# Performance work log

Measured on AMD Instinct MI355X. Metric: run time of the kernel, lower is better.

## Reference

```python
import jax, jax.numpy as jnp
import numpy as np

D_MODEL = 128
NUM_HEADS = 4
D_HEAD = 32
ATTN_COEFF = 0.5
BATCH = 2
SEQ = 4096


def setup_inputs() -> dict:
    key = jax.random.key(0)
    k1, k2, k3, k4, k5 = jax.random.split(key, 5)
    std = 1.0 / np.sqrt(D_MODEL)
    x = jax.random.normal(k1, (BATCH, SEQ, D_MODEL), dtype=jnp.float32)
    W_K = jax.random.normal(k2, (NUM_HEADS, D_HEAD, D_MODEL), dtype=jnp.float32) * std
    W_Q = jax.random.normal(k3, (NUM_HEADS, D_HEAD, D_MODEL), dtype=jnp.float32) * std
    W_V = jax.random.normal(k4, (NUM_HEADS, D_HEAD, D_MODEL), dtype=jnp.float32) * std
    W_O = jax.random.normal(k5, (D_MODEL, NUM_HEADS * D_HEAD), dtype=jnp.float32) * std
    return {"x": x, "W_K": W_K, "W_Q": W_Q, "W_V": W_V, "W_O": W_O}


def reference(x, W_K, W_Q, W_V, W_O):
    batch, seq, _ = x.shape
    # projections: [B, H, S, Dh]
    k = jnp.einsum('ihd,bpd->biph', W_K, x)
    q = jnp.einsum('ihd,bpd->biph', W_Q, x)
    v = jnp.einsum('ihd,bpd->biph', W_V, x)
    # scores: [B, H, Sq, Sk]
    scores = jnp.einsum('biph,biqh->biqp', k, q) / np.sqrt(D_HEAD).astype(np.float32)
    # NOTE: original code builds a causal mask but never applies it; faithful omission.
    attn = jax.nn.softmax(scores, axis=-1)
    # post-softmax affine blend with uniform offset
    attn = attn * ATTN_COEFF + (1.0 - ATTN_COEFF)
    z = jnp.einsum('biph,biqp->biqh', v, attn)          # [B, H, S, Dh]
    z_flat = jnp.transpose(z, (0, 2, 1, 3)).reshape(batch, seq, NUM_HEADS * D_HEAD)
    out = jnp.einsum('df,bpf->bpd', W_O, z_flat)        # [B, S, D]
    return out
```

## Files before the change

kernel.cpp:

```cpp
#include <hip/hip_runtime.h>

#define SQ 4096
#define NB 2
#define NH 4
#define DH 32
#define DM 128

typedef float f32x16 __attribute__((ext_vector_type(16)));
typedef float f32x4  __attribute__((ext_vector_type(4)));
typedef __bf16 bf16x8 __attribute__((ext_vector_type(8)));
typedef unsigned int uint4v __attribute__((ext_vector_type(4)));
typedef unsigned short u16;

union B8 { uint4v u; bf16x8 b; };

__device__ inline u16 f2bf(float x) {
  unsigned u = __builtin_bit_cast(unsigned, x);
  unsigned r = (u + 0x7FFF + ((u >> 16) & 1)) >> 16;
  return (u16)r;
}

__device__ inline unsigned cvt_pk_bf16(float a, float b) {
  unsigned r;
  asm("v_cvt_pk_bf16_f32 %0, %1, %2" : "=v"(r) : "v"(a), "v"(b));
  return r;
}

__device__ inline void swap32(unsigned &a, unsigned &b) {
  asm("v_permlane32_swap_b32 %0, %1" : "+v"(a), "+v"(b));
}

#if __has_builtin(__builtin_amdgcn_exp2f)
#define EX2 __builtin_amdgcn_exp2f
#else
#define EX2 exp2f
#endif

__device__ inline float xhalf_add(float x) {
  unsigned ua = __builtin_bit_cast(unsigned, x), ub = ua;
  asm("v_permlane32_swap_b32 %0, %1" : "+v"(ua), "+v"(ub));
  return __builtin_bit_cast(float, ua) + __builtin_bit_cast(float, ub);
}

__device__ inline bf16x8 ld_cvt8(const float* p) {
  f32x4 a = *(const f32x4*)p;
  f32x4 b = *(const f32x4*)(p + 4);
  B8 r;
  r.u[0] = cvt_pk_bf16(a[0], a[1]);
  r.u[1] = cvt_pk_bf16(a[2], a[3]);
  r.u[2] = cvt_pk_bf16(b[0], b[1]);
  r.u[3] = cvt_pk_bf16(b[2], b[3]);
  return r.b;
}

__global__ __launch_bounds__(256) void kprep(const float* __restrict__ x,
                                             const float* __restrict__ Wo,
                                             u16* __restrict__ wob,
                                             float* __restrict__ xsum) {
  const int bid = blockIdx.x, t = threadIdx.x;
  if (bid < 256) {
    const int b = bid >> 7, rblk = bid & 127;
    const int d = t & 127, rh = t >> 7;
    const float* xp = x + ((size_t)b * SQ + rblk * 32) * DM + d;
    float a = 0.f;
    for (int r = rh; r < 32; r += 2) a += xp[(size_t)r * DM];
    __shared__ float red[2][DM];
    red[rh][d] = a;
    __syncthreads();
    if (t < DM) atomicAdd(&xsum[b * DM + t], red[0][t] + red[1][t]);
  } else {
    for (int i = t; i < DM * DM; i += 256) wob[i] = f2bf(Wo[i]);
  }
}

__global__ __launch_bounds__(256) void kprojc(const float* __restrict__ x,
                                              const float* __restrict__ Wk,
                                              const float* __restrict__ Wq,
                                              const float* __restrict__ Wv,
                                              const float* __restrict__ Wo,
                                              const float* __restrict__ xsum,
                                              u16* __restrict__ qb,
                                              u16* __restrict__ kb,
                                              u16* __restrict__ vt,
                                              float* __restrict__ cvec) {
  const int by = blockIdx.y;
  const int t = threadIdx.x;
  if (by == 12) {
    if (blockIdx.x >= NB) return;
    const int b = blockIdx.x;
    __shared__ float xs[DM], vs[DM];
    if (t < DM) xs[t] = xsum[b * DM + t];
    __syncthreads();
    const int c = t >> 1, half = t & 1;
    float a = 0.f;
    const float* wr = Wv + c * DM + half * 64;
    const float* xh = xs + half * 64;
    for (int i = 0; i < 64; ++i) a += wr[i] * xh[i];
    a += __shfl_xor(a, 1, 64);
    if (half == 0) vs[c] = a;
    __syncthreads();
    float a2 = 0.f;
    const float* wr2 = Wo + c * DM + half * 64;
    const float* vh = vs + half * 64;
    for (int i = 0; i < 64; ++i) a2 += wr2[i] * vh[i];
    a2 += __shfl_xor(a2, 1, 64);
    if (half == 0) cvec[b * DM + c] = 0.5f * a2;
    return;
  }
  const int lane = t & 63, wid = t >> 6;
  const int l31 = lane & 31, hi = lane >> 5;
  const int mat = by >> 2, h = by & 3;
  const int p0 = (blockIdx.x * 4 + wid) * 32;
  const float* xrow = x + (size_t)(p0 + l31) * DM + 8 * hi;
  const float* W = (mat == 0) ? Wk : (mat == 1 ? Wq : Wv);
  const float* wrow = W + (h * 32 + l31) * DM + 8 * hi;
  f32x16 acc;
#pragma unroll
  for (int r = 0; r < 16; ++r) acc[r] = 0.f;
#pragma unroll
  for (int ks = 0; ks < 8; ++ks) {
    bf16x8 af = ld_cvt8(xrow + ks * 16);
    bf16x8 wf = ld_cvt8(wrow + ks * 16);
    acc = __builtin_amdgcn_mfma_f32_32x32x16_bf16(af, wf, acc, 0, 0, 0);
  }
  const float QS = 1.4426950408889634f / 5.656854249492380f;
  const int b = p0 >> 12, pl = p0 & (SQ - 1);
  const size_t bh = (size_t)b * NH + h;
  if (mat == 0) {
    u16* dst = kb + (bh * SQ + pl) * DH + l31;
#pragma unroll
    for (int r = 0; r < 16; ++r) {
      int row = (r & 3) + 8 * (r >> 2) + 4 * hi;
      dst[(size_t)row * DH] = f2bf(acc[r]);
    }
  } else if (mat == 1) {
    u16* dst = qb + (bh * SQ + pl) * DH + l31;
#pragma unroll
    for (int r = 0; r < 16; ++r) {
      int row = (r & 3) + 8 * (r >> 2) + 4 * hi;
      dst[(size_t)row * DH] = f2bf(acc[r] * QS);
    }
  } else {
    u16* dst = vt + ((bh * (SQ / 32) + (pl >> 5)) * DH + l31) * 32;
#pragma unroll
    for (int r = 0; r < 16; ++r) {
      int row = (r & 3) + 8 * (r >> 2) + 4 * hi;
      dst[row] = f2bf(acc[r]);
    }
  }
}

#define TILE(K0, K1, V0, V1, NOFF) {                                               \
  __builtin_amdgcn_s_setprio(1);                                                   \
  f32x16 sc = __builtin_amdgcn_mfma_f32_32x32x16_bf16(K0.b, qf0.b, zacc, 0, 0, 0); \
  sc = __builtin_amdgcn_mfma_f32_32x32x16_bf16(K1.b, qf1.b, sc, 0, 0, 0);          \
  __builtin_amdgcn_s_setprio(0);                                                   \
  K0.u = *(const uint4v*)(kT + (NOFF));                                            \
  K1.u = *(const uint4v*)(kT + (NOFF) + 16);                                       \
  float p_[16];                                                                    \
  _Pragma("unroll") for (int r = 0; r < 16; ++r) p_[r] = EX2(sc[r]);               \
  float ls = ((p_[0]+p_[1])+(p_[2]+p_[3]))+((p_[4]+p_[5])+(p_[6]+p_[7]));          \
  ls += ((p_[8]+p_[9])+(p_[10]+p_[11]))+((p_[12]+p_[13])+(p_[14]+p_[15]));         \
  s += ls;                                                                         \
  unsigned w0 = cvt_pk_bf16(p_[0], p_[1]),  w1 = cvt_pk_bf16(p_[2], p_[3]);        \
  unsigned w2 = cvt_pk_bf16(p_[4], p_[5]),  w3 = cvt_pk_bf16(p_[6], p_[7]);        \
  unsigned w4 = cvt_pk_bf16(p_[8], p_[9]),  w5 = cvt_pk_bf16(p_[10], p_[11]);      \
  unsigned w6 = cvt_pk_bf16(p_[12], p_[13]), w7 = cvt_pk_bf16(p_[14], p_[15]);     \
  swap32(w0, w2); swap32(w1, w3); swap32(w4, w6); swap32(w5, w7);                  \
  B8 bp0_, bp1_;                                                                   \
  bp0_.u[0] = w0; bp0_.u[1] = w1; bp0_.u[2] = w2; bp0_.u[3] = w3;                  \
  bp1_.u[0] = w4; bp1_.u[1] = w5; bp1_.u[2] = w6; bp1_.u[3] = w7;                  \
  __builtin_amdgcn_s_setprio(1);                                                   \
  acc = __builtin_amdgcn_mfma_f32_32x32x16_bf16(V0.b, bp0_.b, acc, 0, 0, 0);       \
  acc = __builtin_amdgcn_mfma_f32_32x32x16_bf16(V1.b, bp1_.b, acc, 0, 0, 0);       \
  __builtin_amdgcn_s_setprio(0);                                                   \
  V0.u = *(const uint4v*)(vT + (NOFF));                                            \
  V1.u = *(const uint4v*)(vT + (NOFF) + 16);                                       \
}

__global__ __launch_bounds__(256, 4) void kattn(const u16* __restrict__ qb,
                                                const u16* __restrict__ kb,
                                                const u16* __restrict__ vt,
                                                u16* __restrict__ yb) {
  __shared__ float ss_[3][64], sa_[3][16][64];
  const int t = threadIdx.x, lane = t & 63, wid = t >> 6;
  const int l31 = lane & 31, hi = lane >> 5;
  const int bh = blockIdx.x & 7;
  const int qbase = (blockIdx.x >> 3) * 32;

  const u16* qrow = qb + ((size_t)bh * SQ + qbase + l31) * DH + 8 * hi;
  B8 qf0, qf1;
  qf0.u = *(const uint4v*)(qrow);
  qf1.u = *(const uint4v*)(qrow + 16);

  const int kh = wid;
  const u16* kT = kb + ((size_t)bh * SQ + kh * 1024) * DH + l31 * 32 + 8 * hi;
  const u16* vT = vt + ((size_t)bh * (SQ / 32) + kh * 32) * (DH * 32) + l31 * 32 + 8 * hi;

  f32x16 zacc, acc;
#pragma unroll
  for (int r = 0; r < 16; ++r) { zacc[r] = -16.f; acc[r] = 0.f; }
  float s = 0.f;

  B8 ka0, ka1, va0, va1, kb0, kb1, vb0, vb1;
  ka0.u = *(const uint4v*)(kT);        ka1.u = *(const uint4v*)(kT + 16);
  va0.u = *(const uint4v*)(vT);        va1.u = *(const uint4v*)(vT + 16);
  kb0.u = *(const uint4v*)(kT + 1024); kb1.u = *(const uint4v*)(kT + 1024 + 16);
  vb0.u = *(const uint4v*)(vT + 1024); vb1.u = *(const uint4v*)(vT + 1024 + 16);

  for (int ti = 0; ti < 32; ti += 2) {
    const int off = ti << 10;
    TILE(ka0, ka1, va0, va1, off + 2048)
    TILE(kb0, kb1, vb0, vb1, off + 3072)
  }

  s = xhalf_add(s);

  if (wid) {
    const int w = wid - 1;
    ss_[w][lane] = s;
#pragma unroll
    for (int r = 0; r < 16; ++r) sa_[w][r][lane] = acc[r];
  }
  __syncthreads();
  if (wid == 0) {
    float den = s;
#pragma unroll
    for (int w = 0; w < 3; ++w) den += ss_[w][lane];
    float inv = 0.5f / den;
    const int b = bh >> 2, h = bh & 3;
    u16* yp = yb + ((size_t)(b * SQ) + qbase + l31) * DM + h * 32;
#pragma unroll
    for (int r = 0; r < 16; ++r) {
      float o = acc[r];
#pragma unroll
      for (int w = 0; w < 3; ++w) o += sa_[w][r][lane];
      int row = (r & 3) + 8 * (r >> 2) + 4 * hi;
      yp[row] = f2bf(o * inv);
    }
  }
}

__global__ __launch_bounds__(256) void kout(const u16* __restrict__ yb,
                                            const u16* __restrict__ wob,
                                            const float* __restrict__ cvec,
                                            float* __restrict__ out) {
  const int t = threadIdx.x, lane = t & 63, wid = t >> 6;
  const int l31 = lane & 31, hi = lane >> 5;
  const int blk = blockIdx.x;
  const int b = blk >> 7;
  const int p0 = (blk & 127) * 32;
  const int d0 = wid * 32;
  const u16* yrow = yb + ((size_t)(b * SQ) + p0 + l31) * DM + 8 * hi;
  const u16* wrow = wob + (size_t)(d0 + l31) * DM + 8 * hi;
  f32x16 acc;
#pragma unroll
  for (int r = 0; r < 16; ++r) acc[r] = 0.f;
#pragma unroll
  for (int ks = 0; ks < 8; ++ks) {
    B8 a, w;
    a.u = *(const uint4v*)(yrow + ks * 16);
    w.u = *(const uint4v*)(wrow + ks * 16);
    acc = __builtin_amdgcn_mfma_f32_32x32x16_bf16(a.b, w.b, acc, 0, 0, 0);
  }
  float cv = cvec[b * DM + d0 + l31];
  float* op = out + ((size_t)(b * SQ) + p0) * DM + d0 + l31;
#pragma unroll
  for (int r = 0; r < 16; ++r) {
    int row = (r & 3) + 8 * (r >> 2) + 4 * hi;
    op[(size_t)row * DM] = acc[r] + cv;
  }
}

extern "C" void kernel_launch(void* const* d_in, const int* in_sizes, int n_in,
                              void* d_out, int out_size, void* d_ws, size_t ws_size,
                              hipStream_t stream) {
  const float* x  = (const float*)d_in[0];
  const float* Wk = (const float*)d_in[1];
  const float* Wq = (const float*)d_in[2];
  const float* Wv = (const float*)d_in[3];
  const float* Wo = (const float*)d_in[4];
  float* out = (float*)d_out;
  char* ws = (char*)d_ws;
  float* xsum = (float*)(ws);
  float* cvec = (float*)(ws + (4 << 10));
  u16* wob = (u16*)(ws + (64 << 10));
  u16* qb = (u16*)(ws + (256 << 10));
  u16* kb = (u16*)(ws + (256 << 10) + ((size_t)2 << 20));
  u16* vt = (u16*)(ws + (256 << 10) + ((size_t)4 << 20));
  u16* yb = (u16*)(ws + (256 << 10) + ((size_t)6 << 20));

  hipMemsetAsync(xsum, 0, NB * DM * sizeof(float), stream);
  kprep<<<dim3(257), dim3(256), 0, stream>>>(x, Wo, wob, xsum);
  kprojc<<<dim3(64, 13), dim3(256), 0, stream>>>(x, Wk, Wq, Wv, Wo, xsum, qb, kb, vt, cvec);
  kattn<<<dim3(1024), dim3(256), 0, stream>>>(qb, kb, vt, yb);
  kout<<<dim3(256), dim3(256), 0, stream>>>(yb, wob, cvec, out);
}
```

Measured before the change: 131.7 us.

## Process two 32-row query tiles per attention block to reuse K/V loads

Each attention block now handles 64 query rows as two 32-row groups that share the same K and V fragments. Each loaded K/V register tile feeds twice the MFMA work, which halves global K/V traffic per query and halves the grid to 512 blocks. In exchange, each thread holds more registers (two accumulators, four Q fragments) and the cross-wave reduction needs twice the shared memory. Fewer blocks on a large GPU may also lower occupancy and parallelism.

```diff
diff --git a/kernel.cpp b/kernel.cpp
--- a/kernel.cpp
+++ b/kernel.cpp
@@ -150,30 +150,37 @@
   }
 }
 
+#define SMPV(SC, S, ACC, V0, V1) {                                              \
+  float p_[16];                                                                 \
+  _Pragma("unroll") for (int r = 0; r < 16; ++r) p_[r] = EX2(SC[r]);            \
+  float ls = ((p_[0]+p_[1])+(p_[2]+p_[3]))+((p_[4]+p_[5])+(p_[6]+p_[7]));       \
+  ls += ((p_[8]+p_[9])+(p_[10]+p_[11]))+((p_[12]+p_[13])+(p_[14]+p_[15]));      \
+  S += ls;                                                                      \
+  unsigned w0 = cvt_pk_bf16(p_[0], p_[1]),  w1 = cvt_pk_bf16(p_[2], p_[3]);     \
+  unsigned w2 = cvt_pk_bf16(p_[4], p_[5]),  w3 = cvt_pk_bf16(p_[6], p_[7]);     \
+  unsigned w4 = cvt_pk_bf16(p_[8], p_[9]),  w5 = cvt_pk_bf16(p_[10], p_[11]);   \
+  unsigned w6 = cvt_pk_bf16(p_[12], p_[13]), w7 = cvt_pk_bf16(p_[14], p_[15]);  \
+  swap32(w0, w2); swap32(w1, w3); swap32(w4, w6); swap32(w5, w7);               \
+  B8 bp0_, bp1_;                                                                \
+  bp0_.u[0] = w0; bp0_.u[1] = w1; bp0_.u[2] = w2; bp0_.u[3] = w3;               \
+  bp1_.u[0] = w4; bp1_.u[1] = w5; bp1_.u[2] = w6; bp1_.u[3] = w7;               \
+  __builtin_amdgcn_s_setprio(1);                                                \
+  ACC = __builtin_amdgcn_mfma_f32_32x32x16_bf16(V0.b, bp0_.b, ACC, 0, 0, 0);    \
+  ACC = __builtin_amdgcn_mfma_f32_32x32x16_bf16(V1.b, bp1_.b, ACC, 0, 0, 0);    \
+  __builtin_amdgcn_s_setprio(0);                                                \
+}
+
 #define TILE(K0, K1, V0, V1, NOFF) {                                               \
   __builtin_amdgcn_s_setprio(1);                                                   \
-  f32x16 sc = __builtin_amdgcn_mfma_f32_32x32x16_bf16(K0.b, qf0.b, zacc, 0, 0, 0); \
-  sc = __builtin_amdgcn_mfma_f32_32x32x16_bf16(K1.b, qf1.b, sc, 0, 0, 0);          \
+  f32x16 sc0 = __builtin_amdgcn_mfma_f32_32x32x16_bf16(K0.b, qf00.b, zacc, 0,0,0); \
+  sc0 = __builtin_amdgcn_mfma_f32_32x32x16_bf16(K1.b, qf01.b, sc0, 0, 0, 0);       \
+  f32x16 sc1 = __builtin_amdgcn_mfma_f32_32x32x16_bf16(K0.b, qf10.b, zacc, 0,0,0); \
+  sc1 = __builtin_amdgcn_mfma_f32_32x32x16_bf16(K1.b, qf11.b, sc1, 0, 0, 0);       \
   __builtin_amdgcn_s_setprio(0);                                                   \
   K0.u = *(const uint4v*)(kT + (NOFF));                                            \
   K1.u = *(const uint4v*)(kT + (NOFF) + 16);                                       \
-  float p_[16];                                                                    \
-  _Pragma("unroll") for (int r = 0; r < 16; ++r) p_[r] = EX2(sc[r]);               \
-  float ls = ((p_[0]+p_[1])+(p_[2]+p_[3]))+((p_[4]+p_[5])+(p_[6]+p_[7]));          \
-  ls += ((p_[8]+p_[9])+(p_[10]+p_[11]))+((p_[12]+p_[13])+(p_[14]+p_[15]));         \
-  s += ls;                                                                         \
-  unsigned w0 = cvt_pk_bf16(p_[0], p_[1]),  w1 = cvt_pk_bf16(p_[2], p_[3]);        \
-  unsigned w2 = cvt_pk_bf16(p_[4], p_[5]),  w3 = cvt_pk_bf16(p_[6], p_[7]);        \
-  unsigned w4 = cvt_pk_bf16(p_[8], p_[9]),  w5 = cvt_pk_bf16(p_[10], p_[11]);      \
-  unsigned w6 = cvt_pk_bf16(p_[12], p_[13]), w7 = cvt_pk_bf16(p_[14], p_[15]);     \
-  swap32(w0, w2); swap32(w1, w3); swap32(w4, w6); swap32(w5, w7);                  \
-  B8 bp0_, bp1_;                                                                   \
-  bp0_.u[0] = w0; bp0_.u[1] = w1; bp0_.u[2] = w2; bp0_.u[3] = w3;                  \
-  bp1_.u[0] = w4; bp1_.u[1] = w5; bp1_.u[2] = w6; bp1_.u[3] = w7;                  \
-  __builtin_amdgcn_s_setprio(1);                                                   \
-  acc = __builtin_amdgcn_mfma_f32_32x32x16_bf16(V0.b, bp0_.b, acc, 0, 0, 0);       \
-  acc = __builtin_amdgcn_mfma_f32_32x32x16_bf16(V1.b, bp1_.b, acc, 0, 0, 0);       \
-  __builtin_amdgcn_s_setprio(0);                                                   \
+  SMPV(sc0, s0, acc0, V0, V1)                                                      \
+  SMPV(sc1, s1, acc1, V0, V1)                                                      \
   V0.u = *(const uint4v*)(vT + (NOFF));                                            \
   V1.u = *(const uint4v*)(vT + (NOFF) + 16);                                       \
 }
@@ -182,25 +189,28 @@
                                                 const u16* __restrict__ kb,
                                                 const u16* __restrict__ vt,
                                                 u16* __restrict__ yb) {
-  __shared__ float ss_[3][64], sa_[3][16][64];
+  __shared__ float ss_[3][2][64], sa_[3][2][16][64];
   const int t = threadIdx.x, lane = t & 63, wid = t >> 6;
   const int l31 = lane & 31, hi = lane >> 5;
   const int bh = blockIdx.x & 7;
-  const int qbase = (blockIdx.x >> 3) * 32;
-
-  const u16* qrow = qb + ((size_t)bh * SQ + qbase + l31) * DH + 8 * hi;
-  B8 qf0, qf1;
-  qf0.u = *(const uint4v*)(qrow);
-  qf1.u = *(const uint4v*)(qrow + 16);
+  const int qbase = (blockIdx.x >> 3) * 64;
+
+  const u16* qrow0 = qb + ((size_t)bh * SQ + qbase + l31) * DH + 8 * hi;
+  const u16* qrow1 = qrow0 + 32 * DH;
+  B8 qf00, qf01, qf10, qf11;
+  qf00.u = *(const uint4v*)(qrow0);
+  qf01.u = *(const uint4v*)(qrow0 + 16);
+  qf10.u = *(const uint4v*)(qrow1);
+  qf11.u = *(const uint4v*)(qrow1 + 16);
 
   const int kh = wid;
   const u16* kT = kb + ((size_t)bh * SQ + kh * 1024) * DH + l31 * 32 + 8 * hi;
   const u16* vT = vt + ((size_t)bh * (SQ / 32) + kh * 32) * (DH * 32) + l31 * 32 + 8 * hi;
 
-  f32x16 zacc, acc;
-#pragma unroll
-  for (int r = 0; r < 16; ++r) { zacc[r] = -16.f; acc[r] = 0.f; }
-  float s = 0.f;
+  f32x16 zacc, acc0, acc1;
+#pragma unroll
+  for (int r = 0; r < 16; ++r) { zacc[r] = -16.f; acc0[r] = 0.f; acc1[r] = 0.f; }
+  float s0 = 0.f, s1 = 0.f;
 
   B8 ka0, ka1, va0, va1, kb0, kb1, vb0, vb1;
   ka0.u = *(const uint4v*)(kT);        ka1.u = *(const uint4v*)(kT + 16);
@@ -214,29 +224,33 @@
     TILE(kb0, kb1, vb0, vb1, off + 3072)
   }
 
-  s = xhalf_add(s);
+  s0 = xhalf_add(s0);
+  s1 = xhalf_add(s1);
 
   if (wid) {
     const int w = wid - 1;
-    ss_[w][lane] = s;
-#pragma unroll
-    for (int r = 0; r < 16; ++r) sa_[w][r][lane] = acc[r];
+    ss_[w][0][lane] = s0; ss_[w][1][lane] = s1;
+#pragma unroll
+    for (int r = 0; r < 16; ++r) { sa_[w][0][r][lane] = acc0[r]; sa_[w][1][r][lane] = acc1[r]; }
   }
   __syncthreads();
   if (wid == 0) {
-    float den = s;
-#pragma unroll
-    for (int w = 0; w < 3; ++w) den += ss_[w][lane];
-    float inv = 0.5f / den;
     const int b = bh >> 2, h = bh & 3;
-    u16* yp = yb + ((size_t)(b * SQ) + qbase + l31) * DM + h * 32;
-#pragma unroll
-    for (int r = 0; r < 16; ++r) {
-      float o = acc[r];
-#pragma unroll
-      for (int w = 0; w < 3; ++w) o += sa_[w][r][lane];
-      int row = (r & 3) + 8 * (r >> 2) + 4 * hi;
-      yp[row] = f2bf(o * inv);
+#pragma unroll
+    for (int g = 0; g < 2; ++g) {
+      float den = g ? s1 : s0;
+#pragma unroll
+      for (int w = 0; w < 3; ++w) den += ss_[w][g][lane];
+      float inv = 0.5f / den;
+      u16* yp = yb + ((size_t)(b * SQ) + qbase + g * 32 + l31) * DM + h * 32;
+#pragma unroll
+      for (int r = 0; r < 16; ++r) {
+        float o = (g ? acc1[r] : acc0[r]);
+#pragma unroll
+        for (int w = 0; w < 3; ++w) o += sa_[w][g][r][lane];
+        int row = (r & 3) + 8 * (r >> 2) + 4 * hi;
+        yp[row] = f2bf(o * inv);
+      }
     }
   }
 }
@@ -293,6 +307,6 @@
   hipMemsetAsync(xsum, 0, NB * DM * sizeof(float), stream);
   kprep<<<dim3(257), dim3(256), 0, stream>>>(x, Wo, wob, xsum);
   kprojc<<<dim3(64, 13), dim3(256), 0, stream>>>(x, Wk, Wq, Wv, Wo, xsum, qb, kb, vt, cvec);
-  kattn<<<dim3(1024), dim3(256), 0, stream>>>(qb, kb, vt, yb);
+  kattn<<<dim3(512), dim3(256), 0, stream>>>(qb, kb, vt, yb);
   kout<<<dim3(256), dim3(256), 0, stream>>>(yb, wob, cvec, out);
 }
```

Result: slower. 346.5 us (+163.2%).

## Share K/V tiles across four query waves via double-buffered LDS async loads

Applied to the files above, without the earlier changes.

Each block now takes 128 queries, one 32-query slice per wave, instead of splitting the key range of 32 queries across waves. K and V tiles are staged into double-buffered LDS with global_load_lds using a swizzled layout, so all four waves reuse each tile. This removes the cross-wave reduction of partial sums through LDS and cuts global K/V traffic by four. The cost is a block-wide barrier every tile, a grid of 256 blocks instead of 1024 (lower occupancy and parallelism), and LDS read latency sitting on the MFMA path.

```diff
diff --git a/kernel.cpp b/kernel.cpp
--- a/kernel.cpp
+++ b/kernel.cpp
@@ -12,6 +12,9 @@
 typedef unsigned int uint4v __attribute__((ext_vector_type(4)));
 typedef unsigned short u16;
 
+#define AS1 __attribute__((address_space(1)))
+#define AS3 __attribute__((address_space(3)))
+
 union B8 { uint4v u; bf16x8 b; };
 
 __device__ inline u16 f2bf(float x) {
@@ -40,6 +43,10 @@
   unsigned ua = __builtin_bit_cast(unsigned, x), ub = ua;
   asm("v_permlane32_swap_b32 %0, %1" : "+v"(ua), "+v"(ub));
   return __builtin_bit_cast(float, ua) + __builtin_bit_cast(float, ub);
+}
+
+__device__ inline void gload16(const void* g, void* l) {
+  __builtin_amdgcn_global_load_lds((const AS1 void*)g, (AS3 void*)l, 16, 0, 0);
 }
 
 __device__ inline bf16x8 ld_cvt8(const float* p) {
@@ -150,13 +157,24 @@
   }
 }
 
-#define TILE(K0, K1, V0, V1, NOFF) {                                               \
+#define STAGE(T, B) {                                              \
+  const char* kg_ = kgbase + (size_t)(T) * 8192;                   \
+  const char* vg_ = vgbase + (size_t)(T) * 8192;                   \
+  gload16(kg_,        &klds[B][woff]);                             \
+  gload16(kg_ + 1024, &klds[B][woff + 1024]);                      \
+  gload16(vg_,        &vlds[B][woff]);                             \
+  gload16(vg_ + 1024, &vlds[B][woff + 1024]);                      \
+}
+
+#define SUB(S) {                                                                   \
+  const int off_ = (S)*2048 + lbase;                                               \
+  B8 k0_, k1_;                                                                     \
+  k0_.u = *(const uint4v*)(kl + off_ + kx0);                                       \
+  k1_.u = *(const uint4v*)(kl + off_ + kx1);                                       \
   __builtin_amdgcn_s_setprio(1);                                                   \
-  f32x16 sc = __builtin_amdgcn_mfma_f32_32x32x16_bf16(K0.b, qf0.b, zacc, 0, 0, 0); \
-  sc = __builtin_amdgcn_mfma_f32_32x32x16_bf16(K1.b, qf1.b, sc, 0, 0, 0);          \
+  f32x16 sc = __builtin_amdgcn_mfma_f32_32x32x16_bf16(k0_.b, qf0.b, zacc, 0,0,0);  \
+  sc = __builtin_amdgcn_mfma_f32_32x32x16_bf16(k1_.b, qf1.b, sc, 0, 0, 0);         \
   __builtin_amdgcn_s_setprio(0);                                                   \
-  K0.u = *(const uint4v*)(kT + (NOFF));                                            \
-  K1.u = *(const uint4v*)(kT + (NOFF) + 16);                                       \
   float p_[16];                                                                    \
   _Pragma("unroll") for (int r = 0; r < 16; ++r) p_[r] = EX2(sc[r]);               \
   float ls = ((p_[0]+p_[1])+(p_[2]+p_[3]))+((p_[4]+p_[5])+(p_[6]+p_[7]));          \
@@ -170,74 +188,66 @@
   B8 bp0_, bp1_;                                                                   \
   bp0_.u[0] = w0; bp0_.u[1] = w1; bp0_.u[2] = w2; bp0_.u[3] = w3;                  \
   bp1_.u[0] = w4; bp1_.u[1] = w5; bp1_.u[2] = w6; bp1_.u[3] = w7;                  \
+  B8 v0_, v1_;                                                                     \
+  v0_.u = *(const uint4v*)(vl + off_ + kx0);                                       \
+  v1_.u = *(const uint4v*)(vl + off_ + kx1);                                       \
   __builtin_amdgcn_s_setprio(1);                                                   \
-  acc = __builtin_amdgcn_mfma_f32_32x32x16_bf16(V0.b, bp0_.b, acc, 0, 0, 0);       \
-  acc = __builtin_amdgcn_mfma_f32_32x32x16_bf16(V1.b, bp1_.b, acc, 0, 0, 0);       \
+  acc = __builtin_amdgcn_mfma_f32_32x32x16_bf16(v0_.b, bp0_.b, acc, 0, 0, 0);      \
+  acc = __builtin_amdgcn_mfma_f32_32x32x16_bf16(v1_.b, bp1_.b, acc, 0, 0, 0);      \
   __builtin_amdgcn_s_setprio(0);                                                   \
-  V0.u = *(const uint4v*)(vT + (NOFF));                                            \
-  V1.u = *(const uint4v*)(vT + (NOFF) + 16);                                       \
-}
-
-__global__ __launch_bounds__(256, 4) void kattn(const u16* __restrict__ qb,
-                                                const u16* __restrict__ kb,
-                                                const u16* __restrict__ vt,
-                                                u16* __restrict__ yb) {
-  __shared__ float ss_[3][64], sa_[3][16][64];
+}
+
+__global__ __launch_bounds__(256) void kattn(const u16* __restrict__ qb,
+                                             const u16* __restrict__ kb,
+                                             const u16* __restrict__ vt,
+                                             u16* __restrict__ yb) {
+  __shared__ char klds[2][8192];
+  __shared__ char vlds[2][8192];
   const int t = threadIdx.x, lane = t & 63, wid = t >> 6;
   const int l31 = lane & 31, hi = lane >> 5;
   const int bh = blockIdx.x & 7;
-  const int qbase = (blockIdx.x >> 3) * 32;
+  const int qbase = (blockIdx.x >> 3) * 128 + wid * 32;
 
   const u16* qrow = qb + ((size_t)bh * SQ + qbase + l31) * DH + 8 * hi;
   B8 qf0, qf1;
   qf0.u = *(const uint4v*)(qrow);
   qf1.u = *(const uint4v*)(qrow + 16);
 
-  const int kh = wid;
-  const u16* kT = kb + ((size_t)bh * SQ + kh * 1024) * DH + l31 * 32 + 8 * hi;
-  const u16* vT = vt + ((size_t)bh * (SQ / 32) + kh * 32) * (DH * 32) + l31 * 32 + 8 * hi;
+  const int srcswz = ((lane >> 2) * 64) + ((((lane & 3) ^ ((lane >> 3) & 3))) << 4);
+  const int woff = wid * 2048;
+  const char* kgbase = (const char*)(kb + (size_t)bh * SQ * DH) + woff + srcswz;
+  const char* vgbase = (const char*)(vt + (size_t)bh * (SQ / 32) * DH * 32) + woff + srcswz;
+
+  const int x_ = (l31 >> 1) & 3;
+  const int kx0 = (hi ^ x_) << 4;
+  const int kx1 = ((2 + hi) ^ x_) << 4;
+  const int lbase = l31 * 64;
 
   f32x16 zacc, acc;
 #pragma unroll
   for (int r = 0; r < 16; ++r) { zacc[r] = -16.f; acc[r] = 0.f; }
   float s = 0.f;
 
-  B8 ka0, ka1, va0, va1, kb0, kb1, vb0, vb1;
-  ka0.u = *(const uint4v*)(kT);        ka1.u = *(const uint4v*)(kT + 16);
-  va0.u = *(const uint4v*)(vT);        va1.u = *(const uint4v*)(vT + 16);
-  kb0.u = *(const uint4v*)(kT + 1024); kb1.u = *(const uint4v*)(kT + 1024 + 16);
-  vb0.u = *(const uint4v*)(vT + 1024); vb1.u = *(const uint4v*)(vT + 1024 + 16);
-
-  for (int ti = 0; ti < 32; ti += 2) {
-    const int off = ti << 10;
-    TILE(ka0, ka1, va0, va1, off + 2048)
-    TILE(kb0, kb1, vb0, vb1, off + 3072)
+  STAGE(0, 0)
+  __syncthreads();
+
+  for (int ti = 0; ti < 32; ++ti) {
+    const int cur = ti & 1;
+    if (ti + 1 < 32) STAGE(ti + 1, cur ^ 1)
+    const char* kl = klds[cur];
+    const char* vl = vlds[cur];
+    SUB(0) SUB(1) SUB(2) SUB(3)
+    __syncthreads();
   }
 
   s = xhalf_add(s);
-
-  if (wid) {
-    const int w = wid - 1;
-    ss_[w][lane] = s;
-#pragma unroll
-    for (int r = 0; r < 16; ++r) sa_[w][r][lane] = acc[r];
-  }
-  __syncthreads();
-  if (wid == 0) {
-    float den = s;
-#pragma unroll
-    for (int w = 0; w < 3; ++w) den += ss_[w][lane];
-    float inv = 0.5f / den;
-    const int b = bh >> 2, h = bh & 3;
-    u16* yp = yb + ((size_t)(b * SQ) + qbase + l31) * DM + h * 32;
-#pragma unroll
-    for (int r = 0; r < 16; ++r) {
-      float o = acc[r];
-#pragma unroll
-      for (int w = 0; w < 3; ++w) o += sa_[w][r][lane];
-      int row = (r & 3) + 8 * (r >> 2) + 4 * hi;
-      yp[row] = f2bf(o * inv);
-    }
+  float inv = 0.5f / s;
+  const int b = bh >> 2, h = bh & 3;
+  u16* yp = yb + ((size_t)(b * SQ) + qbase + l31) * DM + h * 32;
+#pragma unroll
+  for (int r = 0; r < 16; ++r) {
+    int row = (r & 3) + 8 * (r >> 2) + 4 * hi;
+    yp[row] = f2bf(acc[r] * inv);
   }
 }
 
@@ -293,6 +303,6 @@
   hipMemsetAsync(xsum, 0, NB * DM * sizeof(float), stream);
   kprep<<<dim3(257), dim3(256), 0, stream>>>(x, Wo, wob, xsum);
   kprojc<<<dim3(64, 13), dim3(256), 0, stream>>>(x, Wk, Wq, Wv, Wo, xsum, qb, kb, vt, cvec);
-  kattn<<<dim3(1024), dim3(256), 0, stream>>>(qb, kb, vt, yb);
+  kattn<<<dim3(256), dim3(256), 0, stream>>>(qb, kb, vt, yb);
   kout<<<dim3(256), dim3(256), 0, stream>>>(yb, wob, cvec, out);
 }
```

After: 145.5 us. +10.5%, slower.
